# Optimization experiments

Hardware: AMD Instinct MI355X
Metric: run time of the kernel (lower is better)

Reference implementation:

```python
import jax, jax.numpy as jnp
import numpy as np

NOISE_WEIGHT = 1.0
CHAMFER_WEIGHT = 0.1
CHUNK = 1024


def _min_dist_chunked(a, b):
    """For each point in a [B,N,3], squared distance to nearest point in b [B,M,3].
    Processed in chunks of CHUNK points of `a` to avoid materializing [B,N,M].
    Returns [B,N]."""
    B, N, _ = a.shape
    b_sq = jnp.sum(b * b, axis=-1)  # [B,M]
    nc = N // CHUNK
    a_chunks = jnp.moveaxis(a.reshape(B, nc, CHUNK, 3), 1, 0)  # [nc,B,CHUNK,3]

    def body(carry, a_c):
        a_sq = jnp.sum(a_c * a_c, axis=-1)  # [B,CHUNK]
        # d[b,i,j] = |a_i|^2 + |b_j|^2 - 2 a_i.b_j
        d = a_sq[:, :, None] + b_sq[:, None, :] - 2.0 * jnp.einsum('bid,bjd->bij', a_c, b)
        d = jnp.maximum(d, 0.0)
        return carry, jnp.min(d, axis=2)  # [B,CHUNK]

    _, mins = jax.lax.scan(body, None, a_chunks)  # [nc,B,CHUNK]
    return jnp.moveaxis(mins, 0, 1).reshape(B, N)


def chamfer_distance(pred, target):
    d_pt = _min_dist_chunked(pred, target)   # [B,N]
    d_tp = _min_dist_chunked(target, pred)   # [B,M]
    return jnp.mean(d_pt, axis=1) + jnp.mean(d_tp, axis=1)  # [B]


def setup_inputs() -> dict:
    key = jax.random.key(0)
    k1, k2, k3, k4 = jax.random.split(key, 4)
    B, N = 8, 16384
    return {
        'predicted_noise': jax.random.normal(k1, (B, N, 3), dtype=jnp.float32),
        'actual_noise': jax.random.normal(k2, (B, N, 3), dtype=jnp.float32),
        'predicted_points_coarse': jax.random.normal(k3, (B, N, 3), dtype=jnp.float32),
        'target_points_coarse': jax.random.normal(k4, (B, N, 3), dtype=jnp.float32),
    }


def reference(predicted_noise, actual_noise, predicted_points_coarse, target_points_coarse):
    noise_loss = jnp.mean(jnp.abs(predicted_noise - actual_noise))
    chamfer_loss = jnp.mean(chamfer_distance(predicted_points_coarse, target_points_coarse))
    total_loss = NOISE_WEIGHT * noise_loss + CHAMFER_WEIGHT * chamfer_loss
    return total_loss
```

## Files before the change

### kernel.cpp

```cpp
#include <hip/hip_runtime.h>
#include <stdint.h>

#define NPTS        16384
#define BATCH       8
#define QPB         128
#define QBLKS       (NPTS / QPB)
#define CHAM_BLOCKS (BATCH * 2 * QBLKS)
#define NOISE_N     (BATCH * NPTS * 3)
#define NOISE_V4    (NOISE_N / 4)
#define NPTS_TOT    (BATCH * NPTS)
#define PACK_BLOCKS (NPTS_TOT / 256)
#define REF_ITERS   (NPTS * 8 / 1024)

#define WS_NOISE_PART 0
#define WS_CHAM_PART  4096
#define WS_TICKET     12288
#define WS_PK_PRED    16384
#define WS_PK_TARG    (WS_PK_PRED + 8 * NPTS_TOT)
#define WS_R_PRED     (WS_PK_TARG + 8 * NPTS_TOT)
#define WS_R_TARG     (WS_R_PRED + 4 * NPTS_TOT)

using halfx4 = __attribute__((ext_vector_type(4))) _Float16;

__device__ __forceinline__ unsigned int f2h(float f) {
  union { _Float16 h; unsigned short s; } v; v.h = (_Float16)f; return v.s;
}
__device__ __forceinline__ float h2f(unsigned short s) {
  union { _Float16 h; unsigned short u; } v; v.u = s; return (float)v.h;
}

#define T_B0(ACC) \
  "v_min3_f32 v32, v32, v33, v34\n\t" \
  "v_min3_f32 v35, v35, v36, v37\n\t" \
  "v_min3_f32 v38, v38, v39, v40\n\t" \
  "v_min3_f32 v41, v41, v42, v43\n\t" \
  "v_min3_f32 v44, v44, v45, v46\n\t" \
  "v_min3_f32 v32, v32, v35, v38\n\t" \
  "v_min3_f32 v41, v41, v44, v47\n\t" \
  "v_min3_f32 " ACC ", " ACC ", v32, v41\n\t"
#define T_B1(ACC) \
  "v_min3_f32 v48, v48, v49, v50\n\t" \
  "v_min3_f32 v51, v51, v52, v53\n\t" \
  "v_min3_f32 v54, v54, v55, v56\n\t" \
  "v_min3_f32 v57, v57, v58, v59\n\t" \
  "v_min3_f32 v60, v60, v61, v62\n\t" \
  "v_min3_f32 v48, v48, v51, v54\n\t" \
  "v_min3_f32 v57, v57, v60, v63\n\t" \
  "v_min3_f32 " ACC ", " ACC ", v48, v57\n\t"

#define CLOB \
  "v16","v17","v18","v19","v20","v21","v22","v23", \
  "v24","v25","v26","v27","v28","v29","v30","v31", \
  "v32","v33","v34","v35","v36","v37","v38","v39", \
  "v40","v41","v42","v43","v44","v45","v46","v47", \
  "v48","v49","v50","v51","v52","v53","v54","v55", \
  "v56","v57","v58","v59","v60","v61","v62","v63"

#define BLOB(A0, A1, SLOT, BASE)                                          \
  asm volatile(                                                           \
    "s_waitcnt vmcnt(3)\n\t"                                              \
    "v_mfma_f32_32x32x8_f16 v[32:47], " A0 ", %[b0], 0\n\t"               \
    T_B1("%[m3]")                                                         \
    "v_mfma_f32_32x32x8_f16 v[48:63], " A0 ", %[b1], 0\n\t"               \
    "s_nop 0\n\t"                                                         \
    T_B0("%[m0]")                                                         \
    "v_mfma_f32_32x32x8_f16 v[32:47], " A1 ", %[b0], 0\n\t"               \
    "s_nop 0\n\t"                                                         \
    T_B1("%[m1]")                                                         \
    "v_mfma_f32_32x32x8_f16 v[48:63], " A1 ", %[b1], 0\n\t"               \
    "global_load_dwordx4 " SLOT ", %[voff], %[base] offset:3072\n\t"      \
    "s_nop 0\n\t"                                                         \
    T_B0("%[m2]")                                                         \
    : [m0]"+v"(m0), [m1]"+v"(m1), [m2]"+v"(m2), [m3]"+v"(m3)              \
    : [b0]"v"(fb0.v), [b1]"v"(fb1.v), [voff]"v"(voff), [base]"s"(BASE)    \
    : "memory", CLOB)

__global__ void pack_noise_kernel(const float* __restrict__ pred,
                                  const float* __restrict__ targ,
                                  const float4* __restrict__ na,
                                  const float4* __restrict__ nb,
                                  ushort4* __restrict__ pk_pred,
                                  ushort4* __restrict__ pk_targ,
                                  float* __restrict__ r_pred,
                                  float* __restrict__ r_targ,
                                  float* __restrict__ part,
                                  unsigned int* __restrict__ ticket) {
  int i = blockIdx.x * 256 + threadIdx.x;
  if (i == 0) *ticket = 0u;
  {
    float x = pred[3*i+0], y = pred[3*i+1], z = pred[3*i+2];
    float s = __builtin_fmaf(x, x, __builtin_fmaf(y, y, z*z));
    pk_pred[i] = make_ushort4((unsigned short)f2h(x), (unsigned short)f2h(y),
                              (unsigned short)f2h(z), (unsigned short)f2h(s));
    r_pred[i] = s;
  }
  {
    float x = targ[3*i+0], y = targ[3*i+1], z = targ[3*i+2];
    float s = __builtin_fmaf(x, x, __builtin_fmaf(y, y, z*z));
    pk_targ[i] = make_ushort4((unsigned short)f2h(x), (unsigned short)f2h(y),
                              (unsigned short)f2h(z), (unsigned short)f2h(s));
    r_targ[i] = s;
  }
  float sn = 0.f;
  if (i < NOISE_V4) {
    float4 pa = na[i], pb = nb[i];
    sn = fabsf(pa.x-pb.x) + fabsf(pa.y-pb.y) + fabsf(pa.z-pb.z) + fabsf(pa.w-pb.w);
  }
  for (int o = 1; o < 64; o <<= 1) sn += __shfl_xor(sn, o);
  __shared__ float ws4[4];
  int lane = threadIdx.x & 63, wv = threadIdx.x >> 6;
  if (lane == 0) ws4[wv] = sn;
  __syncthreads();
  if (threadIdx.x == 0) part[blockIdx.x] = ws4[0] + ws4[1] + ws4[2] + ws4[3];
}

__global__ __launch_bounds__(256, 4)
void chamfer_kernel(const ushort4* __restrict__ pk_pred,
                    const ushort4* __restrict__ pk_targ,
                    const float* __restrict__ r_pred,
                    const float* __restrict__ r_targ,
                    float* __restrict__ part,
                    const float* __restrict__ part_noise,
                    unsigned int* __restrict__ ticket,
                    float* __restrict__ out) {
  __shared__ float wsum[4];
  __shared__ float flagv;

  const int tid  = threadIdx.x;
  const int lane = tid & 63;
  const int wv   = tid >> 6;
  const int col  = lane & 31;

  const int blk  = blockIdx.x;
  const int qblk = blk & (QBLKS - 1);
  const int bd   = blk >> 7;
  const int dir  = bd & 1;
  const int b    = bd >> 1;

  const ushort4* qpk = dir ? pk_targ : pk_pred;
  const float*   qr  = dir ? r_targ  : r_pred;
  const ushort4* ref = dir ? pk_pred : pk_targ;
  qpk += b * NPTS; qr += b * NPTS; ref += b * NPTS;

  const int q = qblk * QPB + wv * 32 + col;
  ushort4 qt = qpk[q];
  unsigned int nx = f2h(-2.f * h2f(qt.x));
  unsigned int ny = f2h(-2.f * h2f(qt.y));
  unsigned int nz = f2h(-2.f * h2f(qt.z));
  unsigned int lo = (ny << 16) | nx;
  unsigned int hi = (0x3C00u << 16) | nz;
  const bool hh = (lane >= 32);

  union BF { halfx4 v; unsigned int u[2]; };
  BF fb0, fb1;
  fb0.u[0] = hh ? 0u : lo; fb0.u[1] = hh ? 0u : hi;
  fb1.u[0] = hh ? lo : 0u; fb1.u[1] = hh ? hi : 0u;

  const unsigned int voff = (unsigned int)(lane * 16);
  const uint64_t ref_u = (uint64_t)(uintptr_t)ref;

  float m0 = 1e30f, m1 = 1e30f, m2 = 1e30f, m3 = 1e30f;

  asm volatile(
    "global_load_dwordx4 v[16:19], %[voff], %[base] offset:0\n\t"
    "global_load_dwordx4 v[20:23], %[voff], %[base] offset:1024\n\t"
    "global_load_dwordx4 v[24:27], %[voff], %[base] offset:2048\n\t"
    "global_load_dwordx4 v[28:31], %[voff], %[base] offset:3072\n\t"
    "v_mov_b32 v48, 0x7e000000\n\t" "v_mov_b32 v49, 0x7e000000\n\t"
    "v_mov_b32 v50, 0x7e000000\n\t" "v_mov_b32 v51, 0x7e000000\n\t"
    "v_mov_b32 v52, 0x7e000000\n\t" "v_mov_b32 v53, 0x7e000000\n\t"
    "v_mov_b32 v54, 0x7e000000\n\t" "v_mov_b32 v55, 0x7e000000\n\t"
    "v_mov_b32 v56, 0x7e000000\n\t" "v_mov_b32 v57, 0x7e000000\n\t"
    "v_mov_b32 v58, 0x7e000000\n\t" "v_mov_b32 v59, 0x7e000000\n\t"
    "v_mov_b32 v60, 0x7e000000\n\t" "v_mov_b32 v61, 0x7e000000\n\t"
    "v_mov_b32 v62, 0x7e000000\n\t" "v_mov_b32 v63, 0x7e000000"
    :: [voff]"v"(voff), [base]"s"(ref_u) : "memory", CLOB);

  uint64_t bp = ref_u + 1024;
  for (int it = 0; it < REF_ITERS; it += 4) {
    BLOB("v[16:17]", "v[18:19]", "v[16:19]", bp);
    BLOB("v[20:21]", "v[22:23]", "v[20:23]", bp + 1024);
    BLOB("v[24:25]", "v[26:27]", "v[24:27]", bp + 2048);
    BLOB("v[28:29]", "v[30:31]", "v[28:31]", bp + 3072);
    bp += 4096;
  }

  asm volatile(
    "s_waitcnt vmcnt(0)\n\t"
    "s_nop 1\n\t"
    T_B1("%[m3]")
    : [m3]"+v"(m3) :: "memory", CLOB);

  float m = fminf(fminf(m0, m1), fminf(m2, m3));

  m = fminf(m, __shfl_xor(m, 32));
  float rq = qr[q];
  float dmin = fmaxf(rq + m, 0.f);
  float v = (lane < 32) ? dmin : 0.f;
  for (int o = 1; o < 32; o <<= 1) v += __shfl_xor(v, o);
  if (lane == 0) wsum[wv] = v;
  __syncthreads();

  if (tid == 0) {
    atomicExch(&part[blk], wsum[0] + wsum[1] + wsum[2] + wsum[3]);
    __threadfence();
    unsigned int t = atomicAdd(ticket, 1u);
    flagv = (t == CHAM_BLOCKS - 1) ? 1.f : 0.f;
  }
  __syncthreads();

  if (flagv != 0.f) {
    float s = 0.f;
    for (int i = tid; i < PACK_BLOCKS; i += 256) s += part_noise[i];
    float c = 0.f;
    for (int i = tid; i < CHAM_BLOCKS; i += 256) c += atomicAdd(&part[i], 0.f);
    float acc = s * (1.f / NOISE_N) + 0.1f * c * (1.f / NPTS_TOT);
    for (int o = 1; o < 64; o <<= 1) acc += __shfl_xor(acc, o);
    __syncthreads();
    if (lane == 0) wsum[wv] = acc;
    __syncthreads();
    if (tid == 0) out[0] = wsum[0] + wsum[1] + wsum[2] + wsum[3];
  }
}

extern "C" void kernel_launch(void* const* d_in, const int* in_sizes, int n_in,
                              void* d_out, int out_size, void* d_ws, size_t ws_size,
                              hipStream_t stream) {
  const float* pn = (const float*)d_in[0];
  const float* an = (const float*)d_in[1];
  const float* pp = (const float*)d_in[2];
  const float* tp = (const float*)d_in[3];

  char* ws = (char*)d_ws;
  float*        noise_part = (float*)(ws + WS_NOISE_PART);
  float*        cham_part  = (float*)(ws + WS_CHAM_PART);
  unsigned int* ticket     = (unsigned int*)(ws + WS_TICKET);
  ushort4*      pk_pred    = (ushort4*)(ws + WS_PK_PRED);
  ushort4*      pk_targ    = (ushort4*)(ws + WS_PK_TARG);
  float*        r_pred     = (float*)(ws + WS_R_PRED);
  float*        r_targ     = (float*)(ws + WS_R_TARG);

  pack_noise_kernel<<<PACK_BLOCKS, 256, 0, stream>>>(pp, tp, (const float4*)pn, (const float4*)an,
                                                     pk_pred, pk_targ, r_pred, r_targ,
                                                     noise_part, ticket);
  chamfer_kernel<<<CHAM_BLOCKS, 256, 0, stream>>>(pk_pred, pk_targ, r_pred, r_targ,
                                                  cham_part, noise_part, ticket, (float*)d_out);
}
```

Baseline: 168.8 us.

## Replace last-block ticket reduction with separate final kernel and raise occupancy bound

Drops the atomic ticket counter and the last-block-done final reduction from the chamfer kernel, writing each block's partial sum plainly and adding a third single-block kernel to combine the noise and chamfer partials. It also raises the chamfer kernel's launch bounds minimum to 8 blocks per CU, which may push the compiler to use fewer registers. This removes the atomic, fence and extra branch from every block, but adds an extra kernel launch and risks register spills in the hand-scheduled MFMA loop.

```diff
diff --git a/kernel.cpp b/kernel.cpp
--- a/kernel.cpp
+++ b/kernel.cpp
@@ -14,7 +14,6 @@
 
 #define WS_NOISE_PART 0
 #define WS_CHAM_PART  4096
-#define WS_TICKET     12288
 #define WS_PK_PRED    16384
 #define WS_PK_TARG    (WS_PK_PRED + 8 * NPTS_TOT)
 #define WS_R_PRED     (WS_PK_TARG + 8 * NPTS_TOT)
@@ -83,10 +82,8 @@
                                   ushort4* __restrict__ pk_targ,
                                   float* __restrict__ r_pred,
                                   float* __restrict__ r_targ,
-                                  float* __restrict__ part,
-                                  unsigned int* __restrict__ ticket) {
+                                  float* __restrict__ part) {
   int i = blockIdx.x * 256 + threadIdx.x;
-  if (i == 0) *ticket = 0u;
   {
     float x = pred[3*i+0], y = pred[3*i+1], z = pred[3*i+2];
     float s = __builtin_fmaf(x, x, __builtin_fmaf(y, y, z*z));
@@ -114,17 +111,13 @@
   if (threadIdx.x == 0) part[blockIdx.x] = ws4[0] + ws4[1] + ws4[2] + ws4[3];
 }
 
-__global__ __launch_bounds__(256, 4)
+__global__ __launch_bounds__(256, 8)
 void chamfer_kernel(const ushort4* __restrict__ pk_pred,
                     const ushort4* __restrict__ pk_targ,
                     const float* __restrict__ r_pred,
                     const float* __restrict__ r_targ,
-                    float* __restrict__ part,
-                    const float* __restrict__ part_noise,
-                    unsigned int* __restrict__ ticket,
-                    float* __restrict__ out) {
+                    float* __restrict__ part) {
   __shared__ float wsum[4];
-  __shared__ float flagv;
 
   const int tid  = threadIdx.x;
   const int lane = tid & 63;
@@ -200,27 +193,25 @@
   for (int o = 1; o < 32; o <<= 1) v += __shfl_xor(v, o);
   if (lane == 0) wsum[wv] = v;
   __syncthreads();
-
-  if (tid == 0) {
-    atomicExch(&part[blk], wsum[0] + wsum[1] + wsum[2] + wsum[3]);
-    __threadfence();
-    unsigned int t = atomicAdd(ticket, 1u);
-    flagv = (t == CHAM_BLOCKS - 1) ? 1.f : 0.f;
-  }
+  if (tid == 0) part[blockIdx.x] = wsum[0] + wsum[1] + wsum[2] + wsum[3];
+}
+
+__global__ void final_kernel(const float* __restrict__ part_noise,
+                             const float* __restrict__ part_cham,
+                             float* __restrict__ out) {
+  __shared__ float red[256];
+  float s = 0.f;
+  for (int i = threadIdx.x; i < PACK_BLOCKS; i += 256) s += part_noise[i];
+  float t = 0.f;
+  for (int i = threadIdx.x; i < CHAM_BLOCKS; i += 256) t += part_cham[i];
+  red[threadIdx.x] = s; __syncthreads();
+  for (int o = 128; o; o >>= 1) { if (threadIdx.x < o) red[threadIdx.x] += red[threadIdx.x + o]; __syncthreads(); }
+  float noise_sum = red[0];
   __syncthreads();
-
-  if (flagv != 0.f) {
-    float s = 0.f;
-    for (int i = tid; i < PACK_BLOCKS; i += 256) s += part_noise[i];
-    float c = 0.f;
-    for (int i = tid; i < CHAM_BLOCKS; i += 256) c += atomicAdd(&part[i], 0.f);
-    float acc = s * (1.f / NOISE_N) + 0.1f * c * (1.f / NPTS_TOT);
-    for (int o = 1; o < 64; o <<= 1) acc += __shfl_xor(acc, o);
-    __syncthreads();
-    if (lane == 0) wsum[wv] = acc;
-    __syncthreads();
-    if (tid == 0) out[0] = wsum[0] + wsum[1] + wsum[2] + wsum[3];
-  }
+  red[threadIdx.x] = t; __syncthreads();
+  for (int o = 128; o; o >>= 1) { if (threadIdx.x < o) red[threadIdx.x] += red[threadIdx.x + o]; __syncthreads(); }
+  if (threadIdx.x == 0)
+    out[0] = noise_sum * (1.f / NOISE_N) + 0.1f * red[0] * (1.f / NPTS_TOT);
 }
 
 extern "C" void kernel_launch(void* const* d_in, const int* in_sizes, int n_in,
@@ -232,17 +223,15 @@
   const float* tp = (const float*)d_in[3];
 
   char* ws = (char*)d_ws;
-  float*        noise_part = (float*)(ws + WS_NOISE_PART);
-  float*        cham_part  = (float*)(ws + WS_CHAM_PART);
-  unsigned int* ticket     = (unsigned int*)(ws + WS_TICKET);
-  ushort4*      pk_pred    = (ushort4*)(ws + WS_PK_PRED);
-  ushort4*      pk_targ    = (ushort4*)(ws + WS_PK_TARG);
-  float*        r_pred     = (float*)(ws + WS_R_PRED);
-  float*        r_targ     = (float*)(ws + WS_R_TARG);
+  float*   noise_part = (float*)(ws + WS_NOISE_PART);
+  float*   cham_part  = (float*)(ws + WS_CHAM_PART);
+  ushort4* pk_pred    = (ushort4*)(ws + WS_PK_PRED);
+  ushort4* pk_targ    = (ushort4*)(ws + WS_PK_TARG);
+  float*   r_pred     = (float*)(ws + WS_R_PRED);
+  float*   r_targ     = (float*)(ws + WS_R_TARG);
 
   pack_noise_kernel<<<PACK_BLOCKS, 256, 0, stream>>>(pp, tp, (const float4*)pn, (const float4*)an,
-                                                     pk_pred, pk_targ, r_pred, r_targ,
-                                                     noise_part, ticket);
-  chamfer_kernel<<<CHAM_BLOCKS, 256, 0, stream>>>(pk_pred, pk_targ, r_pred, r_targ,
-                                                  cham_part, noise_part, ticket, (float*)d_out);
-}
+                                                     pk_pred, pk_targ, r_pred, r_targ, noise_part);
+  chamfer_kernel<<<CHAM_BLOCKS, 256, 0, stream>>>(pk_pred, pk_targ, r_pred, r_targ, cham_part);
+  final_kernel<<<1, 256, 0, stream>>>(noise_part, cham_part, (float*)d_out);
+}
```

Measured after the change: 152.6 us. -9.6%, faster.
